# Optimization experiments

Hardware: AMD Instinct MI355X
Metric: run time of the kernel (lower is better)

Reference implementation:

```python
import jax, jax.numpy as jnp
import numpy as np

NTOKEN = 150000   # len(ui2idx)
NINP   = 64       # opt.d_word_vec
NHID   = 2 * NINP # gnn1 output dim
NEDGE  = 2400000  # hetero static graph edges
B, L   = 64, 200  # batch_size, max_len


def setup_inputs() -> dict:
    key = jax.random.key(0)
    ks = jax.random.split(key, 8)
    def xavier(k, shape):
        scale = (2.0 / (shape[0] + shape[1])) ** 0.5
        return scale * jax.random.normal(k, shape, jnp.float32)
    emb = xavier(ks[0], (NTOKEN, NINP)).at[0].set(0.0)  # padding_idx=0
    W1 = xavier(ks[1], (NINP, NHID))
    b1 = jnp.zeros((NHID,), jnp.float32)
    W2 = xavier(ks[2], (NHID, NINP))
    b2 = jnp.zeros((NINP,), jnp.float32)
    edge_index = jax.random.randint(ks[3], (2, NEDGE), 0, NTOKEN, dtype=jnp.int32).astype(jnp.int64)
    inp = jax.random.randint(ks[4], (B, L), 0, NTOKEN, dtype=jnp.int32).astype(jnp.int64)
    input_timestamp = jax.random.randint(ks[5], (B, L), 0, 300000, dtype=jnp.int32).astype(jnp.int64)
    return {"emb": emb, "W1": W1, "b1": b1, "W2": W2, "b2": b2,
            "input": inp, "input_timestamp": input_timestamp, "edge_index": edge_index}


def gcn_conv(x, W, b, src, dst, n):
    # torch_geometric GCNConv: out = D^{-1/2}(A+I)D^{-1/2} (x W) + b
    h = x @ W                                   # [n, out]
    deg = jnp.zeros((n,), h.dtype).at[dst].add(1.0) + 1.0  # +1 self-loop
    dinv = jax.lax.rsqrt(deg)
    norm = dinv[src] * dinv[dst]                # [E]
    agg = jax.ops.segment_sum(h[src] * norm[:, None], dst, num_segments=n)
    return agg + h * (dinv * dinv)[:, None] + b  # self-loop term + bias


def reference(emb, W1, b1, W2, b2, input, input_timestamp, edge_index):
    src, dst = edge_index[0], edge_index[1]
    h = gcn_conv(emb, W1, b1, src, dst, NTOKEN)      # dropout is identity in eval
    nodes = gcn_conv(h, W2, b2, src, dst, NTOKEN)    # [NTOKEN, NINP]
    # one-hot scatter + einsum 'bt,td->bd' == direct gather
    b_, l_ = input.shape
    return nodes[input.reshape(-1)].reshape(b_, l_, NINP)
```

## Files before the change

### kernel.cpp

```cpp
#include <hip/hip_runtime.h>
#include <hip/hip_bf16.h>

#define NTOKEN 150000
#define NINP   64
#define NEDGE  2400000
#define NPOS   (64*200)

#define NPB    256
#define NBUCK  586
#define EPB    8192
#define NBLK   293
#define CAP    4608

#define NXB    1172

#define O_XBF      0
#define O_Z1       4800000
#define O_HIST     4800000
#define O_BUCK     9600000
#define O_CTOT     12000000
#define O_BST      12000640
#define O_DINV     12001280
#define O_RS       12151296
#define O_RE       12301312
#define O_M        12451328
#define O_CVEC     12455424

__device__ __forceinline__ unsigned f2bf(float f) {
    unsigned u = __float_as_uint(f);
    return (u + 0x7FFFu + ((u >> 16) & 1u)) >> 16;
}

__global__ void __launch_bounds__(1024) k1(
        const float4* __restrict__ X4, uint4* __restrict__ Xbf,
        const int4* __restrict__ dst4, int* __restrict__ histG,
        const float* __restrict__ W1, const float* __restrict__ b1,
        const float* __restrict__ W2, float* __restrict__ M,
        float* __restrict__ cvec) {
    __shared__ int h[NBUCK];
    int t = threadIdx.x, B = blockIdx.x;
    if (B < NXB) {
        int i = B * 1024 + t;
        if (i < NTOKEN * 64 / 8) {
            float4 a = X4[2 * i], b = X4[2 * i + 1];
            uint4 o;
            o.x = f2bf(a.x) | (f2bf(a.y) << 16);
            o.y = f2bf(a.z) | (f2bf(a.w) << 16);
            o.z = f2bf(b.x) | (f2bf(b.y) << 16);
            o.w = f2bf(b.z) | (f2bf(b.w) << 16);
            Xbf[i] = o;
        }
    } else if (B < NXB + NBLK) {
        int hb = B - NXB;
        for (int i = t; i < NBUCK; i += 1024) h[i] = 0;
        __syncthreads();
        int base4 = hb * (EPB / 4);
        #pragma unroll
        for (int it = 0; it < EPB / 4096; it++) {
            int idx = base4 + it * 1024 + t;
            if (idx < NEDGE / 4) {
                int4 d = dst4[idx];
                atomicAdd(&h[d.x >> 8], 1);
                atomicAdd(&h[d.y >> 8], 1);
                atomicAdd(&h[d.z >> 8], 1);
                atomicAdd(&h[d.w >> 8], 1);
            }
        }
        __syncthreads();
        for (int i = t; i < NBUCK; i += 1024) histG[hb * NBUCK + i] = h[i];
    } else if (B < NXB + NBLK + 4) {
        int o = (B - NXB - NBLK) * 1024 + t;
        int i = o >> 6, j = o & 63;
        float s = 0.f;
        #pragma unroll 4
        for (int k = 0; k < 128; k++) s = fmaf(W1[i * 128 + k], W2[k * 64 + j], s);
        M[o] = s;
    } else if (t < 64) {
        float s = 0.f;
        #pragma unroll 4
        for (int k = 0; k < 128; k++) s = fmaf(b1[k], W2[k * 64 + t], s);
        cvec[t] = s;
    }
}

__global__ void kB1_colscan(int* __restrict__ histG, int* __restrict__ colTotal) {
    __shared__ int sd[256];
    int t = threadIdx.x, b = blockIdx.x;
    int i0 = 2 * t, i1 = 2 * t + 1;
    int v0 = (i0 < NBLK) ? histG[i0 * NBUCK + b] : 0;
    int v1 = (i1 < NBLK) ? histG[i1 * NBUCK + b] : 0;
    int tsum = v0 + v1;
    sd[t] = tsum;
    __syncthreads();
    for (int off = 1; off < 256; off <<= 1) {
        int x = (t >= off) ? sd[t - off] : 0;
        __syncthreads();
        sd[t] += x;
        __syncthreads();
    }
    int excl = sd[t] - tsum;
    if (i0 < NBLK) histG[i0 * NBUCK + b] = excl;
    if (i1 < NBLK) histG[i1 * NBUCK + b] = excl + v0;
    if (t == 255) colTotal[b] = sd[255];
}

__global__ void __launch_bounds__(1024) kC_scatter(
        const int4* __restrict__ src4, const int4* __restrict__ dst4,
        const int* __restrict__ histG, const int* __restrict__ colTotal,
        int* __restrict__ bsG, int* __restrict__ bucketPacked) {
    __shared__ int sd[1024];
    __shared__ int bs[NBUCK + 1];
    __shared__ int cur[NBUCK];
    int t = threadIdx.x, B = blockIdx.x;
    int v0 = (t < NBUCK) ? colTotal[t] : 0;
    sd[t] = v0;
    __syncthreads();
    for (int off = 1; off < 1024; off <<= 1) {
        int x = (t >= off) ? sd[t - off] : 0;
        __syncthreads();
        sd[t] += x;
        __syncthreads();
    }
    if (t < NBUCK) bs[t] = sd[t] - v0;
    if (t == 0) bs[NBUCK] = NEDGE;
    __syncthreads();
    if (B == 0)
        for (int i = t; i < NBUCK + 1; i += 1024) bsG[i] = bs[i];
    for (int i = t; i < NBUCK; i += 1024) cur[i] = histG[B * NBUCK + i] + bs[i];
    __syncthreads();
    int base4 = B * (EPB / 4);
    #pragma unroll
    for (int it = 0; it < EPB / 4096; it++) {
        int idx = base4 + it * 1024 + t;
        if (idx < NEDGE / 4) {
            int4 s = src4[idx];
            int4 d = dst4[idx];
            int p0 = atomicAdd(&cur[d.x >> 8], 1);
            bucketPacked[p0] = (s.x << 8) | (d.x & 255);
            int p1 = atomicAdd(&cur[d.y >> 8], 1);
            bucketPacked[p1] = (s.y << 8) | (d.y & 255);
            int p2 = atomicAdd(&cur[d.z >> 8], 1);
            bucketPacked[p2] = (s.z << 8) | (d.z & 255);
            int p3 = atomicAdd(&cur[d.w >> 8], 1);
            bucketPacked[p3] = (s.w << 8) | (d.w & 255);
        }
    }
}

__global__ void kDp(const int* __restrict__ bsG, const int* __restrict__ packed,
                    float* __restrict__ dinv, int* __restrict__ rowStart,
                    int* __restrict__ rowEnd) {
    __shared__ int cnt[NPB];
    __shared__ int sd[NPB];
    int t = threadIdx.x, b = blockIdx.x;
    int e0 = bsG[b], e1 = bsG[b + 1], nE = e1 - e0;
    if (t < NPB) cnt[t] = 0;
    __syncthreads();
    for (int i = t; i < nE; i += 512) atomicAdd(&cnt[packed[e0 + i] & 255], 1);
    __syncthreads();
    int c = 0;
    if (t < NPB) { c = cnt[t]; sd[t] = c; }
    __syncthreads();
    for (int off = 1; off < 256; off <<= 1) {
        int x = 0;
        if (t < NPB && t >= off) x = sd[t - off];
        __syncthreads();
        if (t < NPB) sd[t] += x;
        __syncthreads();
    }
    if (t < NPB) {
        int excl = sd[t] - c;
        int node = b * NPB + t;
        if (node < NTOKEN) {
            dinv[node] = rsqrtf((float)c + 1.0f);
            rowStart[node] = e0 + excl;
            rowEnd[node]   = e0 + excl + c;
        }
    }
}

__global__ void __launch_bounds__(512) k_agg(
        const uint2* __restrict__ Xb, const float* __restrict__ dinv,
        const int* __restrict__ bsG, const int* __restrict__ rowStart,
        const int* __restrict__ rowEnd,
        int* __restrict__ packed ,
        uint2* __restrict__ Z1b) {
    __shared__ int srt[CAP];
    __shared__ int cur[NPB];
    int t = threadIdx.x, b = blockIdx.x;
    int e0 = bsG[b], e1 = bsG[b + 1], nE = e1 - e0;
    int node = b * NPB + t;
    if (t < NPB) cur[t] = (node < NTOKEN) ? (rowStart[node] - e0) : nE;
    __syncthreads();
    for (int i = t; i < nE; i += 512) {
        int p = packed[e0 + i];
        int pos = atomicAdd(&cur[p & 255], 1);
        if (pos < CAP) srt[pos] = p >> 8;
    }
    __syncthreads();
    for (int i = t; i < nE; i += 512) packed[e0 + i] = srt[i];
    int g = t >> 4, fl = t & 15;
    for (int j = 0; j < 8; j++) {
        int v = b * NPB + g * 8 + j;
        if (v >= NTOKEN) break;
        int ls = rowStart[v] - e0, le = rowEnd[v] - e0;
        float dv = dinv[v];
        uint2 xsw = Xb[(size_t)v * 16 + fl];
        float a0x=0.f,a0y=0.f,a0z=0.f,a0w=0.f, a1x=0.f,a1y=0.f,a1z=0.f,a1w=0.f;
        float a2x=0.f,a2y=0.f,a2z=0.f,a2w=0.f, a3x=0.f,a3y=0.f,a3z=0.f,a3w=0.f;
        for (int e = ls; e < le; e += 8) {
            int m1=e+1<le, m2=e+2<le, m3=e+3<le, m4=e+4<le, m5=e+5<le, m6=e+6<le, m7=e+7<le;
            int u0 = srt[e];
            int u1 = srt[m1 ? e+1 : e];
            int u2 = srt[m2 ? e+2 : e];
            int u3 = srt[m3 ? e+3 : e];
            int u4 = srt[m4 ? e+4 : e];
            int u5 = srt[m5 ? e+5 : e];
            int u6 = srt[m6 ? e+6 : e];
            int u7 = srt[m7 ? e+7 : e];
            float d0 = dinv[u0];
            float d1 = m1 ? dinv[u1] : 0.f;
            float d2 = m2 ? dinv[u2] : 0.f;
            float d3 = m3 ? dinv[u3] : 0.f;
            float d4 = m4 ? dinv[u4] : 0.f;
            float d5 = m5 ? dinv[u5] : 0.f;
            float d6 = m6 ? dinv[u6] : 0.f;
            float d7 = m7 ? dinv[u7] : 0.f;
            uint2 w0 = Xb[(size_t)u0 * 16 + fl];
            uint2 w1 = Xb[(size_t)u1 * 16 + fl];
            uint2 w2 = Xb[(size_t)u2 * 16 + fl];
            uint2 w3 = Xb[(size_t)u3 * 16 + fl];
            uint2 w4 = Xb[(size_t)u4 * 16 + fl];
            uint2 w5 = Xb[(size_t)u5 * 16 + fl];
            uint2 w6 = Xb[(size_t)u6 * 16 + fl];
            uint2 w7 = Xb[(size_t)u7 * 16 + fl];
            #define ACC(d,w,AX,AY,AZ,AW) \
                AX = fmaf(d, __uint_as_float((w).x << 16), AX); \
                AY = fmaf(d, __uint_as_float((w).x & 0xFFFF0000u), AY); \
                AZ = fmaf(d, __uint_as_float((w).y << 16), AZ); \
                AW = fmaf(d, __uint_as_float((w).y & 0xFFFF0000u), AW);
            ACC(d0,w0,a0x,a0y,a0z,a0w)
            ACC(d1,w1,a1x,a1y,a1z,a1w)
            ACC(d2,w2,a2x,a2y,a2z,a2w)
            ACC(d3,w3,a3x,a3y,a3z,a3w)
            ACC(d4,w4,a0x,a0y,a0z,a0w)
            ACC(d5,w5,a1x,a1y,a1z,a1w)
            ACC(d6,w6,a2x,a2y,a2z,a2w)
            ACC(d7,w7,a3x,a3y,a3z,a3w)
            #undef ACC
        }
        float ax = (a0x + a1x) + (a2x + a3x);
        float ay = (a0y + a1y) + (a2y + a3y);
        float az = (a0z + a1z) + (a2z + a3z);
        float aw = (a0w + a1w) + (a2w + a3w);
        float c = dv * dv;
        float ox = c * fmaf(dv, __uint_as_float(xsw.x << 16),         ax);
        float oy = c * fmaf(dv, __uint_as_float(xsw.x & 0xFFFF0000u), ay);
        float oz = c * fmaf(dv, __uint_as_float(xsw.y << 16),         az);
        float ow = c * fmaf(dv, __uint_as_float(xsw.y & 0xFFFF0000u), aw);
        uint2 o;
        o.x = f2bf(ox) | (f2bf(oy) << 16);
        o.y = f2bf(oz) | (f2bf(ow) << 16);
        Z1b[(size_t)v * 16 + fl] = o;
    }
}

__global__ void k_out(const int* __restrict__ inp, const uint2* __restrict__ Z1b,
                      const float* __restrict__ dinv, const int* __restrict__ rowStart,
                      const int* __restrict__ rowEnd, const int* __restrict__ sortedSrc,
                      const float* __restrict__ M, const float* __restrict__ cvec,
                      const float* __restrict__ b2, float* __restrict__ out) {
    int wid = threadIdx.x >> 6;
    int lane = threadIdx.x & 63;
    int g = lane >> 4, fl = lane & 15;
    int p = blockIdx.x * 4 + wid;
    if (p >= NPOS) return;
    int v = inp[p];
    int e0 = rowStart[v], e1 = rowEnd[v];
    float ax0=0.f,ay0=0.f,az0=0.f,aw0=0.f,ss0=0.f;
    float ax1=0.f,ay1=0.f,az1=0.f,aw1=0.f,ss1=0.f;
    int e = e0 + g;
    for (; e + 4 < e1; e += 8) {
        int u0 = sortedSrc[e];
        int u1 = sortedSrc[e + 4];
        ss0 += dinv[u0]; ss1 += dinv[u1];
        uint2 z0 = Z1b[(size_t)u0 * 16 + fl];
        uint2 z1 = Z1b[(size_t)u1 * 16 + fl];
        ax0 += __uint_as_float(z0.x << 16);
        ay0 += __uint_as_float(z0.x & 0xFFFF0000u);
        az0 += __uint_as_float(z0.y << 16);
        aw0 += __uint_as_float(z0.y & 0xFFFF0000u);
        ax1 += __uint_as_float(z1.x << 16);
        ay1 += __uint_as_float(z1.x & 0xFFFF0000u);
        az1 += __uint_as_float(z1.y << 16);
        aw1 += __uint_as_float(z1.y & 0xFFFF0000u);
    }
    if (e < e1) {
        int u = sortedSrc[e];
        ss0 += dinv[u];
        uint2 z = Z1b[(size_t)u * 16 + fl];
        ax0 += __uint_as_float(z.x << 16);
        ay0 += __uint_as_float(z.x & 0xFFFF0000u);
        az0 += __uint_as_float(z.y << 16);
        aw0 += __uint_as_float(z.y & 0xFFFF0000u);
    }
    float ax = ax0 + ax1, ay = ay0 + ay1, az = az0 + az1, aw = aw0 + aw1, ss = ss0 + ss1;
    ax += __shfl_xor(ax, 16, 64); ay += __shfl_xor(ay, 16, 64);
    az += __shfl_xor(az, 16, 64); aw += __shfl_xor(aw, 16, 64);
    ss += __shfl_xor(ss, 16, 64);
    ax += __shfl_xor(ax, 32, 64); ay += __shfl_xor(ay, 32, 64);
    az += __shfl_xor(az, 32, 64); aw += __shfl_xor(aw, 32, 64);
    ss += __shfl_xor(ss, 32, 64);
    float dv = dinv[v];
    uint2 zs = Z1b[(size_t)v * 16 + fl];
    float z2x = dv * (ax + __uint_as_float(zs.x << 16));
    float z2y = dv * (ay + __uint_as_float(zs.x & 0xFFFF0000u));
    float z2z = dv * (az + __uint_as_float(zs.y << 16));
    float z2w = dv * (aw + __uint_as_float(zs.y & 0xFFFF0000u));
    float s = dv * (ss + dv);
    float o = fmaf(s, cvec[lane], b2[lane]);
    #pragma unroll
    for (int kb = 0; kb < 16; kb++) {
        float a0 = __shfl(z2x, kb, 64);
        float a1 = __shfl(z2y, kb, 64);
        float a2 = __shfl(z2z, kb, 64);
        float a3 = __shfl(z2w, kb, 64);
        o = fmaf(a0, M[(kb * 4 + 0) * 64 + lane], o);
        o = fmaf(a1, M[(kb * 4 + 1) * 64 + lane], o);
        o = fmaf(a2, M[(kb * 4 + 2) * 64 + lane], o);
        o = fmaf(a3, M[(kb * 4 + 3) * 64 + lane], o);
    }
    out[(size_t)p * 64 + lane] = o;
}

extern "C" void kernel_launch(void* const* d_in, const int* in_sizes, int n_in,
                              void* d_out, int out_size, void* d_ws, size_t ws_size,
                              hipStream_t stream) {
    const float* emb = (const float*)d_in[0];
    const float* W1  = (const float*)d_in[1];
    const float* b1  = (const float*)d_in[2];
    const float* W2  = (const float*)d_in[3];
    const float* b2  = (const float*)d_in[4];
    const int*   inp = (const int*)d_in[5];
    const int*   ei  = (const int*)d_in[7];
    const int* srcArr = ei;
    const int* dstArr = ei + NEDGE;
    float* out = (float*)d_out;

    float* ws         = (float*)d_ws;
    uint2* Xbf        = (uint2*)(ws + O_XBF);
    uint2* Z1b        = (uint2*)(ws + O_Z1);
    int*   histG      = (int*)ws + O_HIST;
    int*   buckPacked = (int*)ws + O_BUCK;
    int*   colTotal   = (int*)ws + O_CTOT;
    int*   bsG        = (int*)ws + O_BST;
    float* dinv       = ws + O_DINV;
    int*   rowStart   = (int*)ws + O_RS;
    int*   rowEnd     = (int*)ws + O_RE;
    float* M          = ws + O_M;
    float* cvec       = ws + O_CVEC;

    k1         <<<NXB + NBLK + 5, 1024, 0, stream>>>((const float4*)emb, (uint4*)Xbf,
                                                     (const int4*)dstArr, histG,
                                                     W1, b1, W2, M, cvec);
    kB1_colscan<<<NBUCK, 256,  0, stream>>>(histG, colTotal);
    kC_scatter <<<NBLK,  1024, 0, stream>>>((const int4*)srcArr, (const int4*)dstArr,
                                            histG, colTotal, bsG, buckPacked);
    kDp        <<<NBUCK, 512,  0, stream>>>(bsG, buckPacked, dinv, rowStart, rowEnd);
    k_agg      <<<NBUCK, 512,  0, stream>>>(Xbf, dinv, bsG, rowStart, rowEnd,
                                            buckPacked, Z1b);
    k_out      <<<NPOS/4, 256, 0, stream>>>(inp, Z1b, dinv, rowStart, rowEnd,
                                            buckPacked, M, cvec, b2, out);
}
```

Measured before the change: 137.0 us.

## Move local sort into degree kernel and run aggregation one node per group

The in-bucket counting sort of source indices moves from the aggregation kernel into the degree/prefix kernel (now 1024 threads), which writes the sorted sources back to global memory. Aggregation becomes a separate fine-grained kernel with one 16-lane group per node over all tokens, reading sorted sources from global instead of shared memory. rowEnd is replaced by rowStart[v+1] with a sentinel. This aims to raise parallelism and load balance in aggregation, at the cost of extra global reads of the sorted index array instead of LDS.

```diff
diff --git a/kernel.cpp b/kernel.cpp
--- a/kernel.cpp
+++ b/kernel.cpp
@@ -22,7 +22,6 @@
 #define O_BST      12000640
 #define O_DINV     12001280
 #define O_RS       12151296
-#define O_RE       12301312
 #define O_M        12451328
 #define O_CVEC     12455424
 
@@ -147,16 +146,19 @@
     }
 }
 
-__global__ void kDp(const int* __restrict__ bsG, const int* __restrict__ packed,
-                    float* __restrict__ dinv, int* __restrict__ rowStart,
-                    int* __restrict__ rowEnd) {
+__global__ void __launch_bounds__(1024) kDS(
+        const int* __restrict__ bsG,
+        int* __restrict__ bucketPacked ,
+        float* __restrict__ dinv, int* __restrict__ rowStart) {
+    __shared__ int srt[CAP];
     __shared__ int cnt[NPB];
     __shared__ int sd[NPB];
     int t = threadIdx.x, b = blockIdx.x;
     int e0 = bsG[b], e1 = bsG[b + 1], nE = e1 - e0;
+    int nEc = (nE < CAP) ? nE : CAP;
     if (t < NPB) cnt[t] = 0;
     __syncthreads();
-    for (int i = t; i < nE; i += 512) atomicAdd(&cnt[packed[e0 + i] & 255], 1);
+    for (int i = t; i < nEc; i += 1024) atomicAdd(&cnt[bucketPacked[e0 + i] & 255], 1);
     __syncthreads();
     int c = 0;
     if (t < NPB) { c = cnt[t]; sd[t] = c; }
@@ -170,113 +172,103 @@
     }
     if (t < NPB) {
         int excl = sd[t] - c;
+        cnt[t] = excl;
         int node = b * NPB + t;
         if (node < NTOKEN) {
             dinv[node] = rsqrtf((float)c + 1.0f);
             rowStart[node] = e0 + excl;
-            rowEnd[node]   = e0 + excl + c;
         }
-    }
-}
-
-__global__ void __launch_bounds__(512) k_agg(
-        const uint2* __restrict__ Xb, const float* __restrict__ dinv,
-        const int* __restrict__ bsG, const int* __restrict__ rowStart,
-        const int* __restrict__ rowEnd,
-        int* __restrict__ packed ,
-        uint2* __restrict__ Z1b) {
-    __shared__ int srt[CAP];
-    __shared__ int cur[NPB];
-    int t = threadIdx.x, b = blockIdx.x;
-    int e0 = bsG[b], e1 = bsG[b + 1], nE = e1 - e0;
-    int node = b * NPB + t;
-    if (t < NPB) cur[t] = (node < NTOKEN) ? (rowStart[node] - e0) : nE;
-    __syncthreads();
-    for (int i = t; i < nE; i += 512) {
-        int p = packed[e0 + i];
-        int pos = atomicAdd(&cur[p & 255], 1);
+        if (b == NBUCK - 1 && t == 0) rowStart[NTOKEN] = NEDGE;
+    }
+    __syncthreads();
+    for (int i = t; i < nEc; i += 1024) {
+        int p = bucketPacked[e0 + i];
+        int pos = atomicAdd(&cnt[p & 255], 1);
         if (pos < CAP) srt[pos] = p >> 8;
     }
     __syncthreads();
-    for (int i = t; i < nE; i += 512) packed[e0 + i] = srt[i];
-    int g = t >> 4, fl = t & 15;
-    for (int j = 0; j < 8; j++) {
-        int v = b * NPB + g * 8 + j;
-        if (v >= NTOKEN) break;
-        int ls = rowStart[v] - e0, le = rowEnd[v] - e0;
-        float dv = dinv[v];
-        uint2 xsw = Xb[(size_t)v * 16 + fl];
-        float a0x=0.f,a0y=0.f,a0z=0.f,a0w=0.f, a1x=0.f,a1y=0.f,a1z=0.f,a1w=0.f;
-        float a2x=0.f,a2y=0.f,a2z=0.f,a2w=0.f, a3x=0.f,a3y=0.f,a3z=0.f,a3w=0.f;
-        for (int e = ls; e < le; e += 8) {
-            int m1=e+1<le, m2=e+2<le, m3=e+3<le, m4=e+4<le, m5=e+5<le, m6=e+6<le, m7=e+7<le;
-            int u0 = srt[e];
-            int u1 = srt[m1 ? e+1 : e];
-            int u2 = srt[m2 ? e+2 : e];
-            int u3 = srt[m3 ? e+3 : e];
-            int u4 = srt[m4 ? e+4 : e];
-            int u5 = srt[m5 ? e+5 : e];
-            int u6 = srt[m6 ? e+6 : e];
-            int u7 = srt[m7 ? e+7 : e];
-            float d0 = dinv[u0];
-            float d1 = m1 ? dinv[u1] : 0.f;
-            float d2 = m2 ? dinv[u2] : 0.f;
-            float d3 = m3 ? dinv[u3] : 0.f;
-            float d4 = m4 ? dinv[u4] : 0.f;
-            float d5 = m5 ? dinv[u5] : 0.f;
-            float d6 = m6 ? dinv[u6] : 0.f;
-            float d7 = m7 ? dinv[u7] : 0.f;
-            uint2 w0 = Xb[(size_t)u0 * 16 + fl];
-            uint2 w1 = Xb[(size_t)u1 * 16 + fl];
-            uint2 w2 = Xb[(size_t)u2 * 16 + fl];
-            uint2 w3 = Xb[(size_t)u3 * 16 + fl];
-            uint2 w4 = Xb[(size_t)u4 * 16 + fl];
-            uint2 w5 = Xb[(size_t)u5 * 16 + fl];
-            uint2 w6 = Xb[(size_t)u6 * 16 + fl];
-            uint2 w7 = Xb[(size_t)u7 * 16 + fl];
-            #define ACC(d,w,AX,AY,AZ,AW) \
-                AX = fmaf(d, __uint_as_float((w).x << 16), AX); \
-                AY = fmaf(d, __uint_as_float((w).x & 0xFFFF0000u), AY); \
-                AZ = fmaf(d, __uint_as_float((w).y << 16), AZ); \
-                AW = fmaf(d, __uint_as_float((w).y & 0xFFFF0000u), AW);
-            ACC(d0,w0,a0x,a0y,a0z,a0w)
-            ACC(d1,w1,a1x,a1y,a1z,a1w)
-            ACC(d2,w2,a2x,a2y,a2z,a2w)
-            ACC(d3,w3,a3x,a3y,a3z,a3w)
-            ACC(d4,w4,a0x,a0y,a0z,a0w)
-            ACC(d5,w5,a1x,a1y,a1z,a1w)
-            ACC(d6,w6,a2x,a2y,a2z,a2w)
-            ACC(d7,w7,a3x,a3y,a3z,a3w)
-            #undef ACC
-        }
-        float ax = (a0x + a1x) + (a2x + a3x);
-        float ay = (a0y + a1y) + (a2y + a3y);
-        float az = (a0z + a1z) + (a2z + a3z);
-        float aw = (a0w + a1w) + (a2w + a3w);
-        float c = dv * dv;
-        float ox = c * fmaf(dv, __uint_as_float(xsw.x << 16),         ax);
-        float oy = c * fmaf(dv, __uint_as_float(xsw.x & 0xFFFF0000u), ay);
-        float oz = c * fmaf(dv, __uint_as_float(xsw.y << 16),         az);
-        float ow = c * fmaf(dv, __uint_as_float(xsw.y & 0xFFFF0000u), aw);
-        uint2 o;
-        o.x = f2bf(ox) | (f2bf(oy) << 16);
-        o.y = f2bf(oz) | (f2bf(ow) << 16);
-        Z1b[(size_t)v * 16 + fl] = o;
-    }
+    for (int i = t; i < nEc; i += 1024) bucketPacked[e0 + i] = srt[i];
+}
+
+__global__ void k_agg(const uint2* __restrict__ Xb, const float* __restrict__ dinv,
+                      const int* __restrict__ rowStart, const int* __restrict__ sortedSrc,
+                      uint2* __restrict__ Z1b) {
+    int g = threadIdx.x >> 4;
+    int fl = threadIdx.x & 15;
+    int v = blockIdx.x * 16 + g;
+    int e0 = rowStart[v], e1 = rowStart[v + 1];
+    float dv = dinv[v];
+    uint2 xsw = Xb[(size_t)v * 16 + fl];
+    float a0x=0.f,a0y=0.f,a0z=0.f,a0w=0.f, a1x=0.f,a1y=0.f,a1z=0.f,a1w=0.f;
+    float a2x=0.f,a2y=0.f,a2z=0.f,a2w=0.f, a3x=0.f,a3y=0.f,a3z=0.f,a3w=0.f;
+    for (int e = e0; e < e1; e += 8) {
+        int m1=e+1<e1, m2=e+2<e1, m3=e+3<e1, m4=e+4<e1, m5=e+5<e1, m6=e+6<e1, m7=e+7<e1;
+        int u0 = sortedSrc[e];
+        int u1 = sortedSrc[m1 ? e+1 : e];
+        int u2 = sortedSrc[m2 ? e+2 : e];
+        int u3 = sortedSrc[m3 ? e+3 : e];
+        int u4 = sortedSrc[m4 ? e+4 : e];
+        int u5 = sortedSrc[m5 ? e+5 : e];
+        int u6 = sortedSrc[m6 ? e+6 : e];
+        int u7 = sortedSrc[m7 ? e+7 : e];
+        float d0 = dinv[u0];
+        float d1 = m1 ? dinv[u1] : 0.f;
+        float d2 = m2 ? dinv[u2] : 0.f;
+        float d3 = m3 ? dinv[u3] : 0.f;
+        float d4 = m4 ? dinv[u4] : 0.f;
+        float d5 = m5 ? dinv[u5] : 0.f;
+        float d6 = m6 ? dinv[u6] : 0.f;
+        float d7 = m7 ? dinv[u7] : 0.f;
+        uint2 w0 = Xb[(size_t)u0 * 16 + fl];
+        uint2 w1 = Xb[(size_t)u1 * 16 + fl];
+        uint2 w2 = Xb[(size_t)u2 * 16 + fl];
+        uint2 w3 = Xb[(size_t)u3 * 16 + fl];
+        uint2 w4 = Xb[(size_t)u4 * 16 + fl];
+        uint2 w5 = Xb[(size_t)u5 * 16 + fl];
+        uint2 w6 = Xb[(size_t)u6 * 16 + fl];
+        uint2 w7 = Xb[(size_t)u7 * 16 + fl];
+        #define ACC(d,w,AX,AY,AZ,AW) \
+            AX = fmaf(d, __uint_as_float((w).x << 16), AX); \
+            AY = fmaf(d, __uint_as_float((w).x & 0xFFFF0000u), AY); \
+            AZ = fmaf(d, __uint_as_float((w).y << 16), AZ); \
+            AW = fmaf(d, __uint_as_float((w).y & 0xFFFF0000u), AW);
+        ACC(d0,w0,a0x,a0y,a0z,a0w)
+        ACC(d1,w1,a1x,a1y,a1z,a1w)
+        ACC(d2,w2,a2x,a2y,a2z,a2w)
+        ACC(d3,w3,a3x,a3y,a3z,a3w)
+        ACC(d4,w4,a0x,a0y,a0z,a0w)
+        ACC(d5,w5,a1x,a1y,a1z,a1w)
+        ACC(d6,w6,a2x,a2y,a2z,a2w)
+        ACC(d7,w7,a3x,a3y,a3z,a3w)
+        #undef ACC
+    }
+    float ax = (a0x + a1x) + (a2x + a3x);
+    float ay = (a0y + a1y) + (a2y + a3y);
+    float az = (a0z + a1z) + (a2z + a3z);
+    float aw = (a0w + a1w) + (a2w + a3w);
+    float c = dv * dv;
+    float ox = c * fmaf(dv, __uint_as_float(xsw.x << 16),         ax);
+    float oy = c * fmaf(dv, __uint_as_float(xsw.x & 0xFFFF0000u), ay);
+    float oz = c * fmaf(dv, __uint_as_float(xsw.y << 16),         az);
+    float ow = c * fmaf(dv, __uint_as_float(xsw.y & 0xFFFF0000u), aw);
+    uint2 o;
+    o.x = f2bf(ox) | (f2bf(oy) << 16);
+    o.y = f2bf(oz) | (f2bf(ow) << 16);
+    Z1b[(size_t)v * 16 + fl] = o;
 }
 
 __global__ void k_out(const int* __restrict__ inp, const uint2* __restrict__ Z1b,
                       const float* __restrict__ dinv, const int* __restrict__ rowStart,
-                      const int* __restrict__ rowEnd, const int* __restrict__ sortedSrc,
-                      const float* __restrict__ M, const float* __restrict__ cvec,
-                      const float* __restrict__ b2, float* __restrict__ out) {
+                      const int* __restrict__ sortedSrc, const float* __restrict__ M,
+                      const float* __restrict__ cvec, const float* __restrict__ b2,
+                      float* __restrict__ out) {
     int wid = threadIdx.x >> 6;
     int lane = threadIdx.x & 63;
     int g = lane >> 4, fl = lane & 15;
     int p = blockIdx.x * 4 + wid;
     if (p >= NPOS) return;
     int v = inp[p];
-    int e0 = rowStart[v], e1 = rowEnd[v];
+    int e0 = rowStart[v], e1 = rowStart[v + 1];
     float ax0=0.f,ay0=0.f,az0=0.f,aw0=0.f,ss0=0.f;
     float ax1=0.f,ay1=0.f,az1=0.f,aw1=0.f,ss1=0.f;
     int e = e0 + g;
@@ -356,7 +348,6 @@
     int*   bsG        = (int*)ws + O_BST;
     float* dinv       = ws + O_DINV;
     int*   rowStart   = (int*)ws + O_RS;
-    int*   rowEnd     = (int*)ws + O_RE;
     float* M          = ws + O_M;
     float* cvec       = ws + O_CVEC;
 
@@ -366,9 +357,8 @@
     kB1_colscan<<<NBUCK, 256,  0, stream>>>(histG, colTotal);
     kC_scatter <<<NBLK,  1024, 0, stream>>>((const int4*)srcArr, (const int4*)dstArr,
                                             histG, colTotal, bsG, buckPacked);
-    kDp        <<<NBUCK, 512,  0, stream>>>(bsG, buckPacked, dinv, rowStart, rowEnd);
-    k_agg      <<<NBUCK, 512,  0, stream>>>(Xbf, dinv, bsG, rowStart, rowEnd,
-                                            buckPacked, Z1b);
-    k_out      <<<NPOS/4, 256, 0, stream>>>(inp, Z1b, dinv, rowStart, rowEnd,
+    kDS        <<<NBUCK, 1024, 0, stream>>>(bsG, buckPacked, dinv, rowStart);
+    k_agg      <<<NTOKEN/16, 256, 0, stream>>>(Xbf, dinv, rowStart, buckPacked, Z1b);
+    k_out      <<<NPOS/4, 256, 0, stream>>>(inp, Z1b, dinv, rowStart,
                                             buckPacked, M, cvec, b2, out);
 }
```

New measurement: 132.6 us. -3.2%, faster.
